# Optimization experiments

Measured on AMD Instinct MI355X. Metric: run time of the kernel, lower is better.

The kernel has to match this reference:

```python
import jax, jax.numpy as jnp
import numpy as np

# Pyramid configuration (mirrors InstancePyramid: init level grid + requested levels)
INIT_SIZE = (200, 200)
LEVEL_SIZES = [(200, 200), (100, 100), (50, 50), (25, 25), (13, 13)]
G = 28            # shared gaussian table side = feature_scale(7) * 4
CTR = 13          # table center index = 7*2 - 1
N_INST = 512


def _gaussian_table():
    # exp(-ln2 * ((x-13)^2 + (y-13)^2) / 7^2), identical to shared_gaussian_masks()
    xs = jnp.arange(G, dtype=jnp.float32)
    d2 = (xs - CTR) ** 2
    return jnp.exp(-jnp.log(jnp.float32(2.0)) * (d2[:, None] + d2[None, :]) / jnp.float32(7 ** 2))


def setup_inputs() -> dict:
    key = jax.random.key(0)
    pos = jax.random.randint(key, (N_INST, 2), 0, INIT_SIZE[0], dtype=jnp.int32)
    shared_mask = _gaussian_table()  # the fixed learnable-free 28x28 gaussian crop source
    return {"pos": pos, "shared_mask": shared_mask}


def _level_masks(shared_mask, pos, level_size):
    # Vectorized form of get_feature_gaussian_mask over all instances.
    H, W = level_size
    H0, W0 = INIT_SIZE
    # get_root_level_pos: round(pos / init_size * req_size)
    lh = jnp.round(pos[:, 0].astype(jnp.float32) / H0 * H).astype(jnp.int32)  # [N]
    lw = jnp.round(pos[:, 1].astype(jnp.float32) / W0 * W).astype(jnp.int32)  # [N]
    # feature pixel (x, y) reads shared_mask[CTR + x - lh, CTR + y - lw] when in [0, 28)
    si = CTR + jnp.arange(H, dtype=jnp.int32)[None, :] - lh[:, None]   # [N, H]
    sj = CTR + jnp.arange(W, dtype=jnp.int32)[None, :] - lw[:, None]   # [N, W]
    vi = (si >= 0) & (si < G)
    vj = (sj >= 0) & (sj < G)
    gi = jnp.clip(si, 0, G - 1)
    gj = jnp.clip(sj, 0, G - 1)
    m = shared_mask[gi[:, :, None], gj[:, None, :]]                    # [N, H, W] gather
    m = m * (vi[:, :, None] & vj[:, None, :]).astype(m.dtype)          # zero outside crop
    return m.reshape(m.shape[0], -1)


def reference(pos, shared_mask):
    # Per-instance gaussian heatmaps scattered into every pyramid level,
    # flattened and concatenated: [N, sum_l H_l*W_l] = [512, 53294]
    outs = [_level_masks(shared_mask, pos, ls) for ls in LEVEL_SIZES]
    return jnp.concatenate(outs, axis=1)
```

## Files before the change

### kernel.cpp

```cpp
#include <hip/hip_runtime.h>


#define G 28
#define CTR 13
#define ROW 53294

template <int H, int W, int BASE>
__device__ __forceinline__ void paint(const float* __restrict__ mask,
                                      float* __restrict__ row,
                                      int lh, int lw) {
  for (int c = threadIdx.x; c < G * G; c += 256) {
    const int si = c / G;
    const int sj = c - si * G;
    const int i = lh + si - CTR;
    const int j = lw + sj - CTR;
    if ((unsigned)i < (unsigned)H && (unsigned)j < (unsigned)W)
      row[BASE + i * W + j] = mask[c];
  }
}

__global__ __launch_bounds__(256) void paint_kernel(
    const int* __restrict__ pos, const float* __restrict__ mask,
    float* __restrict__ out) {
  const int inst = blockIdx.x;
  const int lvl  = blockIdx.y;

  const int p0 = pos[2 * inst];
  const int p1 = pos[2 * inst + 1];
  const float x0 = (float)p0 * 0.005f;
  const float x1 = (float)p1 * 0.005f;

  float* row = out + (size_t)inst * ROW;
  switch (lvl) {
    case 0: paint<200, 200, 0>(mask, row,
              (int)rintf(x0 * 200.0f), (int)rintf(x1 * 200.0f)); break;
    case 1: paint<100, 100, 40000>(mask, row,
              (int)rintf(x0 * 100.0f), (int)rintf(x1 * 100.0f)); break;
    case 2: paint<50, 50, 50000>(mask, row,
              (int)rintf(x0 * 50.0f), (int)rintf(x1 * 50.0f)); break;
    case 3: paint<25, 25, 52500>(mask, row,
              (int)rintf(x0 * 25.0f), (int)rintf(x1 * 25.0f)); break;
    default: paint<13, 13, 53125>(mask, row,
              (int)rintf(x0 * 13.0f), (int)rintf(x1 * 13.0f)); break;
  }
}

extern "C" void kernel_launch(void* const* d_in, const int* in_sizes, int n_in,
                              void* d_out, int out_size, void* d_ws, size_t ws_size,
                              hipStream_t stream) {
  const int* pos = (const int*)d_in[0];
  const float* mask = (const float*)d_in[1];
  float* out = (float*)d_out;

  hipMemsetAsync(out, 0, (size_t)out_size * sizeof(float), stream);

  dim3 pgrid(512, 5);
  paint_kernel<<<pgrid, 256, 0, stream>>>(pos, mask, out);
}
```

Baseline: 117.7 us.

## Fuse zero-fill into paint kernel, one block per instance

The separate hipMemsetAsync is removed. Each block now zeroes its own instance row with float4 stores, synchronises, then paints all five pyramid levels. This drops one launch and keeps the zero and paint writes to the same row within one block. The cost is fewer blocks (512 instead of 2560) and a serial paint over the five levels per block, and it relies on row+2 being 16-byte aligned (ROW is even, so rows are 8-byte aligned and the +2 offset fixes that).

```diff
diff --git a/kernel.cpp b/kernel.cpp
--- a/kernel.cpp
+++ b/kernel.cpp
@@ -4,6 +4,7 @@
 #define G 28
 #define CTR 13
 #define ROW 53294
+#define BODY_F4 13323
 
 template <int H, int W, int BASE>
 __device__ __forceinline__ void paint(const float* __restrict__ mask,
@@ -19,30 +20,35 @@
   }
 }
 
-__global__ __launch_bounds__(256) void paint_kernel(
+__global__ __launch_bounds__(256) void fused_kernel(
     const int* __restrict__ pos, const float* __restrict__ mask,
     float* __restrict__ out) {
   const int inst = blockIdx.x;
-  const int lvl  = blockIdx.y;
+  float* row = out + (size_t)inst * ROW;
+
+  if (threadIdx.x == 0) *(float2*)row = make_float2(0.f, 0.f);
+  float4* body = (float4*)(row + 2);
+  const float4 z = make_float4(0.f, 0.f, 0.f, 0.f);
+  for (int i = threadIdx.x; i < BODY_F4; i += 256)
+    body[i] = z;
+
+  __syncthreads();
 
   const int p0 = pos[2 * inst];
   const int p1 = pos[2 * inst + 1];
   const float x0 = (float)p0 * 0.005f;
   const float x1 = (float)p1 * 0.005f;
 
-  float* row = out + (size_t)inst * ROW;
-  switch (lvl) {
-    case 0: paint<200, 200, 0>(mask, row,
-              (int)rintf(x0 * 200.0f), (int)rintf(x1 * 200.0f)); break;
-    case 1: paint<100, 100, 40000>(mask, row,
-              (int)rintf(x0 * 100.0f), (int)rintf(x1 * 100.0f)); break;
-    case 2: paint<50, 50, 50000>(mask, row,
-              (int)rintf(x0 * 50.0f), (int)rintf(x1 * 50.0f)); break;
-    case 3: paint<25, 25, 52500>(mask, row,
-              (int)rintf(x0 * 25.0f), (int)rintf(x1 * 25.0f)); break;
-    default: paint<13, 13, 53125>(mask, row,
-              (int)rintf(x0 * 13.0f), (int)rintf(x1 * 13.0f)); break;
-  }
+  paint<200, 200, 0>(mask, row,
+      (int)rintf(x0 * 200.0f), (int)rintf(x1 * 200.0f));
+  paint<100, 100, 40000>(mask, row,
+      (int)rintf(x0 * 100.0f), (int)rintf(x1 * 100.0f));
+  paint<50, 50, 50000>(mask, row,
+      (int)rintf(x0 * 50.0f),  (int)rintf(x1 * 50.0f));
+  paint<25, 25, 52500>(mask, row,
+      (int)rintf(x0 * 25.0f),  (int)rintf(x1 * 25.0f));
+  paint<13, 13, 53125>(mask, row,
+      (int)rintf(x0 * 13.0f),  (int)rintf(x1 * 13.0f));
 }
 
 extern "C" void kernel_launch(void* const* d_in, const int* in_sizes, int n_in,
@@ -52,8 +58,5 @@
   const float* mask = (const float*)d_in[1];
   float* out = (float*)d_out;
 
-  hipMemsetAsync(out, 0, (size_t)out_size * sizeof(float), stream);
-
-  dim3 pgrid(512, 5);
-  paint_kernel<<<pgrid, 256, 0, stream>>>(pos, mask, out);
+  fused_kernel<<<512, 256, 0, stream>>>(pos, mask, out);
 }
```

After: 116.0 us. About the same (-1.5%).
